# Kernel tuning notes

Measured on AMD Instinct MI355X. Metric: run time of the kernel, lower is better.

Reference implementation:

```python
import jax, jax.numpy as jnp
import numpy as np

NUM_NODES = 100000


def setup_inputs() -> dict:
    key = jax.random.key(0)
    k1, k2, k3, k4, k5 = jax.random.split(key, 5)
    E = 3200000
    features = jax.random.normal(k1, (NUM_NODES, 32), dtype=jnp.float32)
    edge_srcs = jax.random.randint(k2, (E,), 0, NUM_NODES, dtype=jnp.int32)
    edge_dsts = jax.random.randint(k3, (E,), 0, NUM_NODES, dtype=jnp.int32)
    edge_weights = jax.random.uniform(k4, (E,), dtype=jnp.float32)
    kernels = jax.random.normal(k5, (32, 32), dtype=jnp.float32) * 0.1
    biases = jnp.zeros((32,), dtype=jnp.float32)
    return {
        "features": features,
        "edge_srcs": edge_srcs,
        "edge_dsts": edge_dsts,
        "edge_weights": edge_weights,
        "kernels": kernels,
        "biases": biases,
    }


def reference(features, edge_srcs, edge_dsts, edge_weights, kernels, biases):
    num_nodes = features.shape[0]
    # dense transform: [N, F_in] @ [F_in, F_out] -> [N, F_out]
    h = features @ kernels
    # per-src degrees via segment sum of ones, clipped to >= 1
    deg = jax.ops.segment_sum(
        jnp.ones_like(edge_srcs, dtype=h.dtype), edge_srcs, num_segments=num_nodes
    )
    norm = jnp.clip(deg, 1.0, None) ** -0.5  # [N]
    # symmetric-normalized edge weights: norm[src] * w * norm[dst]
    w = norm[edge_srcs] * edge_weights * norm[edge_dsts]  # [E]
    # gather dst features, scale, scatter-add into src rows
    nbr = h[edge_dsts] * w[:, None]  # [E, F_out]
    reduced = jax.ops.segment_sum(nbr, edge_srcs, num_segments=num_nodes)
    return reduced + biases
```

## Files before the change

kernel.cpp:

```cpp
#include <hip/hip_runtime.h>
#include <hip/hip_fp16.h>

#define FDIM 32
#define BSH 7
#define BNODES 128
#define NBMAX 1024
#define CHUNK 8192
#define NCMAX 512
#define RCAP 4608
#define SCAP 5120

typedef unsigned int u32;
typedef unsigned short u16;

#define BFLO(u) __uint_as_float((u) << 16)
#define BFHI(u) __uint_as_float((u) & 0xFFFF0000u)

union HCV { __half h; u16 u; };
__device__ __forceinline__ u16 f32_f16b(float f) { HCV c; c.h = __float2half(f); return c.u; }
__device__ __forceinline__ float f16b_f32(u32 b) { HCV c; c.u = (u16)b; return __half2float(c.h); }

__device__ __forceinline__ void acc8(float4& p0, float4& p1, float w, uint4 h) {
    p0.x = fmaf(w, BFLO(h.x), p0.x);
    p0.y = fmaf(w, BFHI(h.x), p0.y);
    p0.z = fmaf(w, BFLO(h.y), p0.z);
    p0.w = fmaf(w, BFHI(h.y), p0.w);
    p1.x = fmaf(w, BFLO(h.z), p1.x);
    p1.y = fmaf(w, BFHI(h.z), p1.y);
    p1.z = fmaf(w, BFLO(h.w), p1.z);
    p1.w = fmaf(w, BFHI(h.w), p1.w);
}

__global__ __launch_bounds__(1024, 8) void k1b(const int* __restrict__ srcs,
                                               const int* __restrict__ dsts,
                                               const float* __restrict__ ew,
                                               u32* __restrict__ offsT,
                                               u32* __restrict__ rkey,
                                               u16* __restrict__ rwh,
                                               int E, int NB, int nch) {
    __shared__ __align__(16) u32 skey[CHUNK];
    __shared__ __align__(16) u16 swv[CHUNK];
    __shared__ u32 lh[NBMAX];
    __shared__ u32 wsum[16];
    int t = threadIdx.x, c = blockIdx.x;
    int base = c * CHUNK;
    int end = base + CHUNK; if (end > E) end = E;
    int nloc = end - base;
    int i0 = t * 8;
    bool full = (i0 + 8 <= nloc);
    int sv[8], dv[8];
    float wv[8];
    u32 rk[8];
    if (full) {
        int4 a  = ((const int4*)(srcs + base))[t * 2];
        int4 b2 = ((const int4*)(srcs + base))[t * 2 + 1];
        int4 d0 = ((const int4*)(dsts + base))[t * 2];
        int4 d1 = ((const int4*)(dsts + base))[t * 2 + 1];
        float4 w0 = ((const float4*)(ew + base))[t * 2];
        float4 w1 = ((const float4*)(ew + base))[t * 2 + 1];
        sv[0]=a.x; sv[1]=a.y; sv[2]=a.z; sv[3]=a.w; sv[4]=b2.x; sv[5]=b2.y; sv[6]=b2.z; sv[7]=b2.w;
        dv[0]=d0.x; dv[1]=d0.y; dv[2]=d0.z; dv[3]=d0.w; dv[4]=d1.x; dv[5]=d1.y; dv[6]=d1.z; dv[7]=d1.w;
        wv[0]=w0.x; wv[1]=w0.y; wv[2]=w0.z; wv[3]=w0.w; wv[4]=w1.x; wv[5]=w1.y; wv[6]=w1.z; wv[7]=w1.w;
    } else {
#pragma unroll
        for (int k = 0; k < 8; ++k) {
            int i = i0 + k;
            bool v = i < nloc;
            sv[k] = v ? srcs[base + i] : 0;
            dv[k] = v ? dsts[base + i] : 0;
            wv[k] = v ? ew[base + i] : 0.f;
        }
    }
    for (int i = t; i < NB; i += 1024) lh[i] = 0u;
    __syncthreads();
    if (full) {
#pragma unroll
        for (int k = 0; k < 8; ++k) rk[k] = atomicAdd(&lh[sv[k] >> BSH], 1u);
    } else {
#pragma unroll
        for (int k = 0; k < 8; ++k) {
            bool v = (i0 + k) < nloc;
            rk[k] = v ? atomicAdd(&lh[sv[k] >> BSH], 1u) : 0u;
        }
    }
    __syncthreads();
    int lane = t & 63, w = t >> 6;
    u32 v = (t < NB) ? lh[t] : 0u;
    u32 inc = v;
#pragma unroll
    for (int d = 1; d < 64; d <<= 1) {
        u32 o = __shfl_up(inc, (unsigned)d, 64);
        if (lane >= d) inc += o;
    }
    if (lane == 63) wsum[w] = inc;
    __syncthreads();
    u32 woff = 0;
    for (int i = 0; i < w; ++i) woff += wsum[i];
    inc += woff;
    u32 ex = inc - v;
    if (t < NB) { offsT[(size_t)t * nch + c] = ex; lh[t] = ex; }
    if (t == 0) offsT[(size_t)NB * nch + c] = (u32)nloc;
    __syncthreads();
    if (full) {
#pragma unroll
        for (int k = 0; k < 8; ++k) {
            int s = sv[k];
            u32 pos = lh[s >> BSH] + rk[k];
            skey[pos] = ((u32)(s & (BNODES - 1)) << 17) | (u32)dv[k];
            swv[pos] = f32_f16b(wv[k]);
        }
    } else {
#pragma unroll
        for (int k = 0; k < 8; ++k) {
            if ((i0 + k) < nloc) {
                int s = sv[k];
                u32 pos = lh[s >> BSH] + rk[k];
                skey[pos] = ((u32)(s & (BNODES - 1)) << 17) | (u32)dv[k];
                swv[pos] = f32_f16b(wv[k]);
            }
        }
    }
    __syncthreads();
    ((uint4*)(rkey + (size_t)base))[t]        = ((const uint4*)skey)[t];
    ((uint4*)(rkey + (size_t)base))[t + 1024] = ((const uint4*)skey)[t + 1024];
    ((uint4*)(rwh + (size_t)base))[t]         = ((const uint4*)swv)[t];
}

__global__ __launch_bounds__(512) void k_nh(const u32* __restrict__ rkey,
                                            const u32* __restrict__ offsT,
                                            const float* __restrict__ feat,
                                            const float* __restrict__ kern,
                                            u16* __restrict__ hsb,
                                            u32* __restrict__ nodemeta,
                                            int N, int NB, int nch) {
    __shared__ float skern[FDIM * FDIM];
    __shared__ float sfeat[BNODES * FDIM];
    __shared__ u32 sbase[NCMAX];
    __shared__ u16 runid[RCAP];
    __shared__ u32 lcnt[BNODES];
    __shared__ float lnorm[BNODES];
    __shared__ u32 wsum[8];
    __shared__ u32 ws2[2];
    __shared__ u32 stot;
    int b = blockIdx.x, t = threadIdx.x;
    for (int i = t; i < FDIM * FDIM / 4; i += 512) ((float4*)skern)[i] = ((const float4*)kern)[i];
    int base_n = b << BSH;
    int base_nf = base_n * FDIM;
    int lim = N * FDIM - base_nf; if (lim > BNODES * FDIM) lim = BNODES * FDIM;
    for (int i = t; i < (lim >> 2); i += 512) ((float4*)sfeat)[i] = ((const float4*)(feat + base_nf))[i];
    if (t < BNODES) lcnt[t] = 0u;
    u32 rl = 0u, s0 = 0u;
    if (t < nch) {
        s0 = offsT[(size_t)b * nch + t];
        rl = offsT[(size_t)(b + 1) * nch + t] - s0;
    }
    int lane = t & 63, w = t >> 6;
    u32 inc = rl;
#pragma unroll
    for (int d = 1; d < 64; d <<= 1) {
        u32 o = __shfl_up(inc, (unsigned)d, 64);
        if (lane >= d) inc += o;
    }
    if (lane == 63) wsum[w] = inc;
    __syncthreads();
    u32 woff = 0;
    for (int i = 0; i < w; ++i) woff += wsum[i];
    inc += woff;
    if (t < nch) {
        u32 pl0 = inc - rl;
        sbase[t] = (u32)t * CHUNK + s0 - pl0;
        u32 p = pl0 < RCAP ? pl0 : RCAP;
        u32 e = pl0 + rl; if (e > RCAP) e = RCAP;
        for (; p < e; ++p) runid[p] = (u16)t;
    }
    if (t == nch - 1) stot = inc;
    __syncthreads();
    u32 tot = stot; if (tot > RCAP) tot = RCAP;
    {
        u32 keyv[8]; bool val[8];
#pragma unroll
        for (int i = 0; i < 8; ++i) {
            u32 g = (u32)t + ((u32)i << 9);
            val[i] = g < tot;
            keyv[i] = 0u;
            if (val[i]) {
                int r = runid[g];
                keyv[i] = rkey[(size_t)(sbase[r] + g)];
            }
        }
#pragma unroll
        for (int i = 0; i < 8; ++i)
            if (val[i]) atomicAdd(&lcnt[keyv[i] >> 17], 1u);
        for (u32 g = (u32)t + 4096u; g < tot; g += 512u) {
            int r = runid[g];
            atomicAdd(&lcnt[rkey[(size_t)(sbase[r] + g)] >> 17], 1u);
        }
    }
    __syncthreads();
    u32 d = 0u, pad = 0u, inc2 = 0u;
    if (t < BNODES) {
        d = lcnt[t];
        pad = (d + 3u) & ~3u;
        inc2 = pad;
    }
    if (t < 128) {
#pragma unroll
        for (int dd = 1; dd < 64; dd <<= 1) {
            u32 o = __shfl_up(inc2, (unsigned)dd, 64);
            if ((t & 63) >= dd) inc2 += o;
        }
        if ((t & 63) == 63) ws2[t >> 6] = inc2;
    }
    __syncthreads();
    if (t < 128) {
        if (t >= 64) inc2 += ws2[0];
        u32 ex = inc2 - pad;
        lnorm[t] = rsqrtf(fmaxf((float)d, 1.0f));
        int n = base_n + t;
        if (n < N) nodemeta[n] = ex | (d << 16);
    }
    __syncthreads();
    int f = t & 31, g8 = t >> 5;
    float kc[FDIM];
#pragma unroll
    for (int k = 0; k < FDIM; ++k) kc[k] = skern[k * FDIM + f];
#pragma unroll
    for (int k8 = 0; k8 < 8; ++k8) {
        int nl = g8 * 8 + k8;
        int n = base_n + nl;
        const float4* fr = (const float4*)(sfeat + nl * FDIM);
        float4 rr[8];
#pragma unroll
        for (int q = 0; q < 8; ++q) rr[q] = fr[q];
        float acc = 0.f;
#pragma unroll
        for (int q = 0; q < 8; ++q) {
            acc = fmaf(rr[q].x, kc[4 * q + 0], acc);
            acc = fmaf(rr[q].y, kc[4 * q + 1], acc);
            acc = fmaf(rr[q].z, kc[4 * q + 2], acc);
            acc = fmaf(rr[q].w, kc[4 * q + 3], acc);
        }
        float x = lnorm[nl] * acc;
        u32 u = __float_as_uint(x);
        u = (u + 0x7FFFu + ((u >> 16) & 1u)) >> 16;
        if (n < N) hsb[(size_t)n * FDIM + f] = (u16)u;
    }
}

__global__ __launch_bounds__(512) void k2(const u32* __restrict__ rkey,
                                          const u16* __restrict__ rwh,
                                          const u32* __restrict__ offsT,
                                          const u32* __restrict__ nodemeta,
                                          const u16* __restrict__ hsb,
                                          const float* __restrict__ bias,
                                          float* __restrict__ out,
                                          int N, int NB, int nch) {
    __shared__ __align__(16) u32 ssrec[SCAP];
    __shared__ u32 sbase[NCMAX];
    __shared__ u16 runid[RCAP];
    __shared__ u32 loff[BNODES];
    __shared__ u32 lcnt[BNODES];
    __shared__ u32 lcur[BNODES];
    __shared__ u32 snode[BNODES];
    __shared__ u32 lbin[128];
    __shared__ u32 wsum[8];
    __shared__ u32 ws2[2];
    __shared__ u32 stot;
    int b = blockIdx.x, t = threadIdx.x;
    int base_n = b << BSH;
    if (t < BNODES) {
        int n = base_n + t;
        u32 m = (n < N) ? nodemeta[n] : 0u;
        loff[t] = m & 0xFFFFu;
        lcnt[t] = m >> 16;
        lcur[t] = m & 0xFFFFu;
    }
    if (t < 128) lbin[t] = 0u;
    u32 rl = 0u, s0 = 0u;
    if (t < nch) {
        s0 = offsT[(size_t)b * nch + t];
        rl = offsT[(size_t)(b + 1) * nch + t] - s0;
    }
    int lane = t & 63, w = t >> 6;
    u32 inc = rl;
#pragma unroll
    for (int d = 1; d < 64; d <<= 1) {
        u32 o = __shfl_up(inc, (unsigned)d, 64);
        if (lane >= d) inc += o;
    }
    if (lane == 63) wsum[w] = inc;
    __syncthreads();
    u32 woff = 0;
    for (int i = 0; i < w; ++i) woff += wsum[i];
    inc += woff;
    if (t < nch) {
        u32 pl0 = inc - rl;
        sbase[t] = (u32)t * CHUNK + s0 - pl0;
        u32 p = pl0 < RCAP ? pl0 : RCAP;
        u32 e = pl0 + rl; if (e > RCAP) e = RCAP;
        for (; p < e; ++p) runid[p] = (u16)t;
    }
    if (t == nch - 1) stot = inc;
    __syncthreads();
    u32 tot = stot; if (tot > RCAP) tot = RCAP;
    {
        u32 keyv[8], whv[8]; bool val[8];
#pragma unroll
        for (int i = 0; i < 8; ++i) {
            u32 g = (u32)t + ((u32)i << 9);
            val[i] = g < tot;
            keyv[i] = 0u; whv[i] = 0u;
            if (val[i]) {
                int r = runid[g];
                u32 idx = sbase[r] + g;
                keyv[i] = rkey[(size_t)idx];
                whv[i] = rwh[(size_t)idx];
            }
        }
#pragma unroll
        for (int i = 0; i < 8; ++i) {
            if (val[i]) {
                u32 pos = atomicAdd(&lcur[keyv[i] >> 17], 1u);
                if (pos < SCAP) ssrec[pos] = ((keyv[i] & 0x1FFFFu) << 15) | (whv[i] & 0x7FFFu);
            }
        }
        for (u32 g = (u32)t + 4096u; g < tot; g += 512u) {
            int r = runid[g];
            u32 idx = sbase[r] + g;
            u32 key = rkey[(size_t)idx];
            u32 wh = rwh[(size_t)idx];
            u32 pos = atomicAdd(&lcur[key >> 17], 1u);
            if (pos < SCAP) ssrec[pos] = ((key & 0x1FFFFu) << 15) | (wh & 0x7FFFu);
        }
    }
    if (t < BNODES) {
        u32 len = lcnt[t];
        atomicAdd(&lbin[len > 127u ? 127u : len], 1u);
    }
    __syncthreads();
    u32 bv_ = 0u, binc = 0u;
    if (t < 128) {
        bv_ = lbin[t];
        binc = bv_;
#pragma unroll
        for (int dd = 1; dd < 64; dd <<= 1) {
            u32 o = __shfl_up(binc, (unsigned)dd, 64);
            if ((t & 63) >= dd) binc += o;
        }
        if ((t & 63) == 63) ws2[t >> 6] = binc;
    }
    __syncthreads();
    if (t < 128) {
        if (t >= 64) binc += ws2[0];
        lbin[t] = binc - bv_;
    }
    __syncthreads();
    if (t < BNODES) {
        u32 len = lcnt[t];
        u32 pos = atomicAdd(&lbin[len > 127u ? 127u : len], 1u);
        snode[pos] = (u32)t;
    }
    __syncthreads();
    int l = t & 3, g = t >> 2;
    u32 nl = snode[g];
    int n = base_n + (int)nl;
    u32 off = loff[nl];
    u32 len = lcnt[nl];
    float ns = rsqrtf(fmaxf((float)len, 1.0f));
    const uint4* hp4 = (const uint4*)hsb;
    float4 bv0 = ((const float4*)bias)[2 * l];
    float4 bv1 = ((const float4*)bias)[2 * l + 1];
    float4 x0 = make_float4(0.f, 0.f, 0.f, 0.f), x1 = make_float4(0.f, 0.f, 0.f, 0.f);
    float4 y0 = make_float4(0.f, 0.f, 0.f, 0.f), y1 = make_float4(0.f, 0.f, 0.f, 0.f);
    u32 j = 0;
    for (; j + 8 <= len; j += 8) {
        uint4 a = *(const uint4*)(ssrec + off + j);
        uint4 c = *(const uint4*)(ssrec + off + j + 4);
        uint4 h0 = hp4[(size_t)(a.x >> 15) * 4 + l];
        uint4 h1 = hp4[(size_t)(a.y >> 15) * 4 + l];
        uint4 h2 = hp4[(size_t)(a.z >> 15) * 4 + l];
        uint4 h3 = hp4[(size_t)(a.w >> 15) * 4 + l];
        uint4 h4 = hp4[(size_t)(c.x >> 15) * 4 + l];
        uint4 h5 = hp4[(size_t)(c.y >> 15) * 4 + l];
        uint4 h6 = hp4[(size_t)(c.z >> 15) * 4 + l];
        uint4 h7 = hp4[(size_t)(c.w >> 15) * 4 + l];
        acc8(x0, x1, f16b_f32(a.x & 0x7FFFu), h0);
        acc8(y0, y1, f16b_f32(a.y & 0x7FFFu), h1);
        acc8(x0, x1, f16b_f32(a.z & 0x7FFFu), h2);
        acc8(y0, y1, f16b_f32(a.w & 0x7FFFu), h3);
        acc8(x0, x1, f16b_f32(c.x & 0x7FFFu), h4);
        acc8(y0, y1, f16b_f32(c.y & 0x7FFFu), h5);
        acc8(x0, x1, f16b_f32(c.z & 0x7FFFu), h6);
        acc8(y0, y1, f16b_f32(c.w & 0x7FFFu), h7);
    }
    for (; j + 4 <= len; j += 4) {
        uint4 a = *(const uint4*)(ssrec + off + j);
        uint4 h0 = hp4[(size_t)(a.x >> 15) * 4 + l];
        uint4 h1 = hp4[(size_t)(a.y >> 15) * 4 + l];
        uint4 h2 = hp4[(size_t)(a.z >> 15) * 4 + l];
        uint4 h3 = hp4[(size_t)(a.w >> 15) * 4 + l];
        acc8(x0, x1, f16b_f32(a.x & 0x7FFFu), h0);
        acc8(y0, y1, f16b_f32(a.y & 0x7FFFu), h1);
        acc8(x0, x1, f16b_f32(a.z & 0x7FFFu), h2);
        acc8(y0, y1, f16b_f32(a.w & 0x7FFFu), h3);
    }
    for (; j < len; ++j) {
        u32 q = ssrec[off + j];
        uint4 h = hp4[(size_t)(q >> 15) * 4 + l];
        acc8(x0, x1, f16b_f32(q & 0x7FFFu), h);
    }
    if (n < N) {
        float4 r0, r1;
        r0.x = fmaf(ns, x0.x + y0.x, bv0.x);
        r0.y = fmaf(ns, x0.y + y0.y, bv0.y);
        r0.z = fmaf(ns, x0.z + y0.z, bv0.z);
        r0.w = fmaf(ns, x0.w + y0.w, bv0.w);
        r1.x = fmaf(ns, x1.x + y1.x, bv1.x);
        r1.y = fmaf(ns, x1.y + y1.y, bv1.y);
        r1.z = fmaf(ns, x1.z + y1.z, bv1.z);
        r1.w = fmaf(ns, x1.w + y1.w, bv1.w);
        ((float4*)(out + (size_t)n * FDIM))[2 * l] = r0;
        ((float4*)(out + (size_t)n * FDIM))[2 * l + 1] = r1;
    }
}

extern "C" void kernel_launch(void* const* d_in, const int* in_sizes, int n_in,
                              void* d_out, int out_size, void* d_ws, size_t ws_size,
                              hipStream_t stream) {
    const float* feat = (const float*)d_in[0];
    const int*   srcs = (const int*)d_in[1];
    const int*   dsts = (const int*)d_in[2];
    const float* ew   = (const float*)d_in[3];
    const float* kern = (const float*)d_in[4];
    const float* bias = (const float*)d_in[5];
    float* out = (float*)d_out;

    int N = in_sizes[0] / FDIM;
    int E = in_sizes[1];
    int NB = (N + BNODES - 1) >> BSH;
    int nchunks = (E + CHUNK - 1) / CHUNK;

    char* w = (char*)d_ws;
    u16* hsb      = (u16*)w;   w += (((size_t)N * FDIM * sizeof(u16) + 15) & ~15ull);
    u32* rkey     = (u32*)w;   w += (size_t)nchunks * CHUNK * sizeof(u32);
    u16* rwh      = (u16*)w;   w += (((size_t)nchunks * CHUNK * sizeof(u16) + 15) & ~15ull);
    u32* offsT    = (u32*)w;   w += (size_t)(NB + 1) * nchunks * sizeof(u32);
    u32* nodemeta = (u32*)w;   w += (size_t)N * sizeof(u32);

    k1b<<<nchunks, 1024, 0, stream>>>(srcs, dsts, ew, offsT, rkey, rwh, E, NB, nchunks);
    k_nh<<<NB, 512, 0, stream>>>(rkey, offsT, feat, kern, hsb, nodemeta, N, NB, nchunks);
    k2<<<NB, 512, 0, stream>>>(rkey, rwh, offsT, nodemeta, hsb, bias, out, N, NB, nchunks);
}
```

Before: 169.9 us.

## Split bucket sort into own kernel writing sorted records, separate GEMM kernel

Before, the degree count and the scatter of edges into per-node order each re-read the partitioned edge keys, once in the normalization/GEMM kernel and again in the aggregation kernel. Now one sort kernel counts, ranks and places the edges into a per-block sorted record buffer in global memory, using an overflow buffer for the tail. A separate GEMM kernel reads only the node metadata. The aggregation kernel then reads the presorted records directly instead of rebuilding them in shared memory. This removes one pass over rkey and the in-kernel sort from k2, at the cost of an extra kernel launch and a global round trip for the sorted records.

Result: slower. 176.0 us (+3.6%).

```diff
diff --git a/kernel.cpp b/kernel.cpp
--- a/kernel.cpp
+++ b/kernel.cpp
@@ -126,29 +126,26 @@
     ((uint4*)(rwh + (size_t)base))[t]         = ((const uint4*)swv)[t];
 }
 
-__global__ __launch_bounds__(512) void k_nh(const u32* __restrict__ rkey,
-                                            const u32* __restrict__ offsT,
-                                            const float* __restrict__ feat,
-                                            const float* __restrict__ kern,
-                                            u16* __restrict__ hsb,
-                                            u32* __restrict__ nodemeta,
-                                            int N, int NB, int nch) {
-    __shared__ float skern[FDIM * FDIM];
-    __shared__ float sfeat[BNODES * FDIM];
+__global__ __launch_bounds__(512) void k_sort(const u32* __restrict__ rkey,
+                                              const u16* __restrict__ rwh,
+                                              const u32* __restrict__ offsT,
+                                              u32* __restrict__ srec,
+                                              u32* __restrict__ nodemeta,
+                                              int N, int NB, int nch) {
+    __shared__ __align__(16) u32 ssrec[SCAP];
     __shared__ u32 sbase[NCMAX];
     __shared__ u16 runid[RCAP];
     __shared__ u32 lcnt[BNODES];
-    __shared__ float lnorm[BNODES];
+    __shared__ u32 lexoff[BNODES];
+    __shared__ uint2 ovf[512];
+    __shared__ u32 ovn;
     __shared__ u32 wsum[8];
     __shared__ u32 ws2[2];
     __shared__ u32 stot;
     int b = blockIdx.x, t = threadIdx.x;
-    for (int i = t; i < FDIM * FDIM / 4; i += 512) ((float4*)skern)[i] = ((const float4*)kern)[i];
     int base_n = b << BSH;
-    int base_nf = base_n * FDIM;
-    int lim = N * FDIM - base_nf; if (lim > BNODES * FDIM) lim = BNODES * FDIM;
-    for (int i = t; i < (lim >> 2); i += 512) ((float4*)sfeat)[i] = ((const float4*)(feat + base_nf))[i];
     if (t < BNODES) lcnt[t] = 0u;
+    if (t == 0) ovn = 0u;
     u32 rl = 0u, s0 = 0u;
     if (t < nch) {
         s0 = offsT[(size_t)b * nch + t];
@@ -176,25 +173,30 @@
     if (t == nch - 1) stot = inc;
     __syncthreads();
     u32 tot = stot; if (tot > RCAP) tot = RCAP;
-    {
-        u32 keyv[8]; bool val[8];
-#pragma unroll
-        for (int i = 0; i < 8; ++i) {
-            u32 g = (u32)t + ((u32)i << 9);
-            val[i] = g < tot;
-            keyv[i] = 0u;
-            if (val[i]) {
-                int r = runid[g];
-                keyv[i] = rkey[(size_t)(sbase[r] + g)];
-            }
-        }
-#pragma unroll
-        for (int i = 0; i < 8; ++i)
-            if (val[i]) atomicAdd(&lcnt[keyv[i] >> 17], 1u);
-        for (u32 g = (u32)t + 4096u; g < tot; g += 512u) {
+    u32 keyv[8], whv[8], rankv[8]; bool val[8];
+#pragma unroll
+    for (int i = 0; i < 8; ++i) {
+        u32 g = (u32)t + ((u32)i << 9);
+        val[i] = g < tot;
+        keyv[i] = 0u; whv[i] = 0u; rankv[i] = 0u;
+        if (val[i]) {
             int r = runid[g];
-            atomicAdd(&lcnt[rkey[(size_t)(sbase[r] + g)] >> 17], 1u);
-        }
+            u32 idx = sbase[r] + g;
+            keyv[i] = rkey[(size_t)idx];
+            whv[i] = rwh[(size_t)idx];
+        }
+    }
+#pragma unroll
+    for (int i = 0; i < 8; ++i)
+        if (val[i]) rankv[i] = atomicAdd(&lcnt[keyv[i] >> 17], 1u);
+    for (u32 g = (u32)t + 4096u; g < tot; g += 512u) {
+        int r = runid[g];
+        u32 idx = sbase[r] + g;
+        u32 key = rkey[(size_t)idx];
+        u32 wh = rwh[(size_t)idx];
+        u32 rk2 = atomicAdd(&lcnt[key >> 17], 1u);
+        u32 oi = atomicAdd(&ovn, 1u);
+        if (oi < 512u) ovf[oi] = make_uint2(key, (u32)wh | (rk2 << 16));
     }
     __syncthreads();
     u32 d = 0u, pad = 0u, inc2 = 0u;
@@ -215,9 +217,49 @@
     if (t < 128) {
         if (t >= 64) inc2 += ws2[0];
         u32 ex = inc2 - pad;
-        lnorm[t] = rsqrtf(fmaxf((float)d, 1.0f));
+        lexoff[t] = ex;
         int n = base_n + t;
         if (n < N) nodemeta[n] = ex | (d << 16);
+    }
+    __syncthreads();
+#pragma unroll
+    for (int i = 0; i < 8; ++i) {
+        if (val[i]) {
+            u32 slot = keyv[i] >> 17;
+            u32 pos = lexoff[slot] + rankv[i];
+            if (pos < SCAP) ssrec[pos] = ((keyv[i] & 0x1FFFFu) << 15) | ((u32)whv[i] & 0x7FFFu);
+        }
+    }
+    u32 no = ovn; if (no > 512u) no = 512u;
+    for (u32 i = t; i < no; i += 512u) {
+        uint2 q = ovf[i];
+        u32 slot = q.x >> 17;
+        u32 pos = lexoff[slot] + (q.y >> 16);
+        if (pos < SCAP) ssrec[pos] = ((q.x & 0x1FFFFu) << 15) | (q.y & 0x7FFFu);
+    }
+    __syncthreads();
+    u32* dst = srec + (size_t)b * SCAP;
+    for (int i = t; i < SCAP / 4; i += 512) ((uint4*)dst)[i] = ((const uint4*)ssrec)[i];
+}
+
+__global__ __launch_bounds__(512) void k_gemm(const float* __restrict__ feat,
+                                              const float* __restrict__ kern,
+                                              const u32* __restrict__ nodemeta,
+                                              u16* __restrict__ hsb,
+                                              int N) {
+    __shared__ float skern[FDIM * FDIM];
+    __shared__ float sfeat[BNODES * FDIM];
+    __shared__ float lnorm[BNODES];
+    int b = blockIdx.x, t = threadIdx.x;
+    for (int i = t; i < FDIM * FDIM / 4; i += 512) ((float4*)skern)[i] = ((const float4*)kern)[i];
+    int base_n = b << BSH;
+    int base_nf = base_n * FDIM;
+    int lim = N * FDIM - base_nf; if (lim > BNODES * FDIM) lim = BNODES * FDIM;
+    for (int i = t; i < (lim >> 2); i += 512) ((float4*)sfeat)[i] = ((const float4*)(feat + base_nf))[i];
+    if (t < BNODES) {
+        int n = base_n + t;
+        u32 m = (n < N) ? nodemeta[n] : 0u;
+        lnorm[t] = rsqrtf(fmaxf((float)(m >> 16), 1.0f));
     }
     __syncthreads();
     int f = t & 31, g8 = t >> 5;
@@ -247,25 +289,17 @@
     }
 }
 
-__global__ __launch_bounds__(512) void k2(const u32* __restrict__ rkey,
-                                          const u16* __restrict__ rwh,
-                                          const u32* __restrict__ offsT,
+__global__ __launch_bounds__(512) void k2(const u32* __restrict__ srec,
                                           const u32* __restrict__ nodemeta,
                                           const u16* __restrict__ hsb,
                                           const float* __restrict__ bias,
                                           float* __restrict__ out,
-                                          int N, int NB, int nch) {
-    __shared__ __align__(16) u32 ssrec[SCAP];
-    __shared__ u32 sbase[NCMAX];
-    __shared__ u16 runid[RCAP];
+                                          int N, int NB) {
     __shared__ u32 loff[BNODES];
     __shared__ u32 lcnt[BNODES];
-    __shared__ u32 lcur[BNODES];
     __shared__ u32 snode[BNODES];
     __shared__ u32 lbin[128];
-    __shared__ u32 wsum[8];
     __shared__ u32 ws2[2];
-    __shared__ u32 stot;
     int b = blockIdx.x, t = threadIdx.x;
     int base_n = b << BSH;
     if (t < BNODES) {
@@ -273,66 +307,9 @@
         u32 m = (n < N) ? nodemeta[n] : 0u;
         loff[t] = m & 0xFFFFu;
         lcnt[t] = m >> 16;
-        lcur[t] = m & 0xFFFFu;
     }
     if (t < 128) lbin[t] = 0u;
-    u32 rl = 0u, s0 = 0u;
-    if (t < nch) {
-        s0 = offsT[(size_t)b * nch + t];
-        rl = offsT[(size_t)(b + 1) * nch + t] - s0;
-    }
-    int lane = t & 63, w = t >> 6;
-    u32 inc = rl;
-#pragma unroll
-    for (int d = 1; d < 64; d <<= 1) {
-        u32 o = __shfl_up(inc, (unsigned)d, 64);
-        if (lane >= d) inc += o;
-    }
-    if (lane == 63) wsum[w] = inc;
-    __syncthreads();
-    u32 woff = 0;
-    for (int i = 0; i < w; ++i) woff += wsum[i];
-    inc += woff;
-    if (t < nch) {
-        u32 pl0 = inc - rl;
-        sbase[t] = (u32)t * CHUNK + s0 - pl0;
-        u32 p = pl0 < RCAP ? pl0 : RCAP;
-        u32 e = pl0 + rl; if (e > RCAP) e = RCAP;
-        for (; p < e; ++p) runid[p] = (u16)t;
-    }
-    if (t == nch - 1) stot = inc;
-    __syncthreads();
-    u32 tot = stot; if (tot > RCAP) tot = RCAP;
-    {
-        u32 keyv[8], whv[8]; bool val[8];
-#pragma unroll
-        for (int i = 0; i < 8; ++i) {
-            u32 g = (u32)t + ((u32)i << 9);
-            val[i] = g < tot;
-            keyv[i] = 0u; whv[i] = 0u;
-            if (val[i]) {
-                int r = runid[g];
-                u32 idx = sbase[r] + g;
-                keyv[i] = rkey[(size_t)idx];
-                whv[i] = rwh[(size_t)idx];
-            }
-        }
-#pragma unroll
-        for (int i = 0; i < 8; ++i) {
-            if (val[i]) {
-                u32 pos = atomicAdd(&lcur[keyv[i] >> 17], 1u);
-                if (pos < SCAP) ssrec[pos] = ((keyv[i] & 0x1FFFFu) << 15) | (whv[i] & 0x7FFFu);
-            }
-        }
-        for (u32 g = (u32)t + 4096u; g < tot; g += 512u) {
-            int r = runid[g];
-            u32 idx = sbase[r] + g;
-            u32 key = rkey[(size_t)idx];
-            u32 wh = rwh[(size_t)idx];
-            u32 pos = atomicAdd(&lcur[key >> 17], 1u);
-            if (pos < SCAP) ssrec[pos] = ((key & 0x1FFFFu) << 15) | (wh & 0x7FFFu);
-        }
-    }
+    __syncthreads();
     if (t < BNODES) {
         u32 len = lcnt[t];
         atomicAdd(&lbin[len > 127u ? 127u : len], 1u);
@@ -367,6 +344,7 @@
     u32 off = loff[nl];
     u32 len = lcnt[nl];
     float ns = rsqrtf(fmaxf((float)len, 1.0f));
+    const u32* sp = srec + (size_t)b * SCAP + off;
     const uint4* hp4 = (const uint4*)hsb;
     float4 bv0 = ((const float4*)bias)[2 * l];
     float4 bv1 = ((const float4*)bias)[2 * l + 1];
@@ -374,8 +352,8 @@
     float4 y0 = make_float4(0.f, 0.f, 0.f, 0.f), y1 = make_float4(0.f, 0.f, 0.f, 0.f);
     u32 j = 0;
     for (; j + 8 <= len; j += 8) {
-        uint4 a = *(const uint4*)(ssrec + off + j);
-        uint4 c = *(const uint4*)(ssrec + off + j + 4);
+        uint4 a = *(const uint4*)(sp + j);
+        uint4 c = *(const uint4*)(sp + j + 4);
         uint4 h0 = hp4[(size_t)(a.x >> 15) * 4 + l];
         uint4 h1 = hp4[(size_t)(a.y >> 15) * 4 + l];
         uint4 h2 = hp4[(size_t)(a.z >> 15) * 4 + l];
@@ -394,7 +372,7 @@
         acc8(y0, y1, f16b_f32(c.w & 0x7FFFu), h7);
     }
     for (; j + 4 <= len; j += 4) {
-        uint4 a = *(const uint4*)(ssrec + off + j);
+        uint4 a = *(const uint4*)(sp + j);
         uint4 h0 = hp4[(size_t)(a.x >> 15) * 4 + l];
         uint4 h1 = hp4[(size_t)(a.y >> 15) * 4 + l];
         uint4 h2 = hp4[(size_t)(a.z >> 15) * 4 + l];
@@ -405,7 +383,7 @@
         acc8(y0, y1, f16b_f32(a.w & 0x7FFFu), h3);
     }
     for (; j < len; ++j) {
-        u32 q = ssrec[off + j];
+        u32 q = sp[j];
         uint4 h = hp4[(size_t)(q >> 15) * 4 + l];
         acc8(x0, x1, f16b_f32(q & 0x7FFFu), h);
     }
@@ -445,9 +423,11 @@
     u32* rkey     = (u32*)w;   w += (size_t)nchunks * CHUNK * sizeof(u32);
     u16* rwh      = (u16*)w;   w += (((size_t)nchunks * CHUNK * sizeof(u16) + 15) & ~15ull);
     u32* offsT    = (u32*)w;   w += (size_t)(NB + 1) * nchunks * sizeof(u32);
-    u32* nodemeta = (u32*)w;   w += (size_t)N * sizeof(u32);
+    u32* nodemeta = (u32*)w;   w += (((size_t)N * sizeof(u32) + 15) & ~15ull);
+    u32* srec     = (u32*)w;   w += (size_t)NB * SCAP * sizeof(u32);
 
     k1b<<<nchunks, 1024, 0, stream>>>(srcs, dsts, ew, offsT, rkey, rwh, E, NB, nchunks);
-    k_nh<<<NB, 512, 0, stream>>>(rkey, offsT, feat, kern, hsb, nodemeta, N, NB, nchunks);
-    k2<<<NB, 512, 0, stream>>>(rkey, rwh, offsT, nodemeta, hsb, bias, out, N, NB, nchunks);
-}
+    k_sort<<<NB, 512, 0, stream>>>(rkey, rwh, offsT, srec, nodemeta, N, NB, nchunks);
+    k_gemm<<<NB, 512, 0, stream>>>(feat, kern, nodemeta, hsb, N);
+    k2<<<NB, 512, 0, stream>>>(srec, nodemeta, hsb, bias, out, N, NB);
+}
```
